# Kernel optimization log

Hardware: AMD Instinct MI355X
Metric: run time of the kernel (lower is better)

## Reference

```python
import jax, jax.numpy as jnp
import numpy as np

B, D, O = 256, 4096, 16384


def setup_inputs() -> dict:
    key = jax.random.key(0)
    k1, k2, k3, k4 = jax.random.split(key, 4)
    x1 = jax.random.normal(k1, (B, D), dtype=jnp.float32)
    x2 = jax.random.normal(k2, (B, D), dtype=jnp.float32)
    # random hash buckets in [0, O) and random +/-1 signs (homogeneous: shared by both inputs)
    h1 = jax.random.randint(k3, (D,), 0, O, dtype=jnp.int32)
    s1 = jnp.where(jax.random.uniform(k4, (D,)) < 0.5, -1.0, 1.0).astype(jnp.float32)
    return {"x1": x1, "x2": x2, "h1": h1, "s1": s1, "output_size": O}


def reference(x1, x2, h1, s1, output_size):
    # psi(): count-sketch via sign-multiply + scatter-add along feature axis
    batch = x1.shape[0]
    y1 = jnp.zeros((batch, output_size), x1.dtype).at[:, h1].add(s1 * x1)  # [B, O]
    y2 = jnp.zeros((batch, output_size), x2.dtype).at[:, h1].add(s1 * x2)  # [B, O]
    # conv(): circular convolution of the two sketches via FFT pointwise product
    out = jnp.fft.ifft(jnp.fft.fft(y1, axis=-1) * jnp.fft.fft(y2, axis=-1), axis=-1)
    return out.real.astype(x1.dtype)
```

## Files before the change

### kernel.cpp

```cpp
#include <hip/hip_runtime.h>


#define FFT_N   16384
#define LOGN    14
#define BLOCK   1024
#define DIM     4096
#define SLOT(e) ((e) ^ (((e) >> 4) & 15))
#define PI_F    3.14159265358979323846f

__device__ __forceinline__ float2 cmul(float2 a, float2 b) {
    return make_float2(a.x * b.x - a.y * b.y, a.x * b.y + a.y * b.x);
}
__device__ __forceinline__ float2 csqr(float2 a) {
    return make_float2(a.x * a.x - a.y * a.y, 2.f * a.x * a.y);
}

__device__ __forceinline__ void fft8_dif(float2* r, float phi) {
    const float CT8[4] = {1.f, 0.70710678f, 0.f, -0.70710678f};
    const float ST8[4] = {0.f, 0.70710678f, 1.f, 0.70710678f};
    float2 W[3];
    __sincosf(phi, &W[2].y, &W[2].x);
    W[1] = csqr(W[2]); W[0] = csqr(W[1]);
    #pragma unroll
    for (int p = 2; p >= 0; --p) {
        #pragma unroll
        for (int h = 0; h < 4; ++h) {
            const int jp = h & ((1 << p) - 1);
            const int j  = ((h >> p) << (p + 1)) | jp;
            const int ci = jp << (2 - p);
            const float2 T = cmul(W[p], make_float2(CT8[ci], -ST8[ci]));
            float2 a = r[j], b = r[j + (1 << p)];
            r[j] = make_float2(a.x + b.x, a.y + b.y);
            float2 d = make_float2(a.x - b.x, a.y - b.y);
            r[j + (1 << p)] = cmul(d, T);
        }
    }
}

__device__ __forceinline__ void fft8_dit(float2* r, float phi) {
    const float CT8[4] = {1.f, 0.70710678f, 0.f, -0.70710678f};
    const float ST8[4] = {0.f, 0.70710678f, 1.f, 0.70710678f};
    float2 W[3];
    __sincosf(phi, &W[2].y, &W[2].x);
    W[1] = csqr(W[2]); W[0] = csqr(W[1]);
    #pragma unroll
    for (int p = 0; p <= 2; ++p) {
        #pragma unroll
        for (int h = 0; h < 4; ++h) {
            const int jp = h & ((1 << p) - 1);
            const int j  = ((h >> p) << (p + 1)) | jp;
            const int ci = jp << (2 - p);
            const float2 T = cmul(W[p], make_float2(CT8[ci], ST8[ci]));
            float2 a = r[j];
            float2 b = cmul(r[j + (1 << p)], T);
            r[j]            = make_float2(a.x + b.x, a.y + b.y);
            r[j + (1 << p)] = make_float2(a.x - b.x, a.y - b.y);
        }
    }
}

__device__ __forceinline__ void fft4_dif(float2* r) {
    float2 a, b, d;
    a = r[0]; b = r[2]; r[0] = make_float2(a.x + b.x, a.y + b.y);
    r[2] = make_float2(a.x - b.x, a.y - b.y);
    a = r[1]; b = r[3]; r[1] = make_float2(a.x + b.x, a.y + b.y);
    d = make_float2(a.x - b.x, a.y - b.y);
    r[3] = make_float2(d.y, -d.x);
    a = r[0]; b = r[1]; r[0] = make_float2(a.x + b.x, a.y + b.y);
    r[1] = make_float2(a.x - b.x, a.y - b.y);
    a = r[2]; b = r[3]; r[2] = make_float2(a.x + b.x, a.y + b.y);
    r[3] = make_float2(a.x - b.x, a.y - b.y);
}

__device__ __forceinline__ void fft4_dit(float2* r) {
    float2 a, b;
    a = r[0]; b = r[1]; r[0] = make_float2(a.x + b.x, a.y + b.y);
    r[1] = make_float2(a.x - b.x, a.y - b.y);
    a = r[2]; b = r[3]; r[2] = make_float2(a.x + b.x, a.y + b.y);
    r[3] = make_float2(a.x - b.x, a.y - b.y);
    a = r[0]; b = r[2]; r[0] = make_float2(a.x + b.x, a.y + b.y);
    r[2] = make_float2(a.x - b.x, a.y - b.y);
    a = r[1]; b = make_float2(-r[3].y, r[3].x);
    r[1] = make_float2(a.x + b.x, a.y + b.y);
    r[3] = make_float2(a.x - b.x, a.y - b.y);
}

__device__ __forceinline__ void pass8_dif(float2* zz, int base, int slog, float phi) {
    float2 r[8];
    #pragma unroll
    for (int j = 0; j < 8; ++j) r[j] = zz[SLOT(base + (j << slog))];
    fft8_dif(r, phi);
    #pragma unroll
    for (int j = 0; j < 8; ++j) zz[SLOT(base + (j << slog))] = r[j];
}
__device__ __forceinline__ void pass8_dit(float2* zz, int base, int slog, float phi) {
    float2 r[8];
    #pragma unroll
    for (int j = 0; j < 8; ++j) r[j] = zz[SLOT(base + (j << slog))];
    fft8_dit(r, phi);
    #pragma unroll
    for (int j = 0; j < 8; ++j) zz[SLOT(base + (j << slog))] = r[j];
}

#define WAVE_FENCE() __asm__ volatile("s_waitcnt lgkmcnt(0)" ::: "memory")

__launch_bounds__(BLOCK, 4)
__global__ void cbp_fft_kernel(const float* __restrict__ x1,
                               const float* __restrict__ x2,
                               const int* __restrict__ h1,
                               const float* __restrict__ s1,
                               float* __restrict__ out) {
    __shared__ float2 zz[FFT_N];
    const int tid = threadIdx.x;
    const int b   = blockIdx.x;

    #pragma unroll
    for (int j = 0; j < 16; ++j) zz[tid + (j << 10)] = make_float2(0.f, 0.f);
    __syncthreads();

    const float* x1r = x1 + (size_t)b * DIM;
    const float* x2r = x2 + (size_t)b * DIM;
    #pragma unroll
    for (int i = 0; i < DIM / BLOCK; ++i) {
        int d = tid + i * BLOCK;
        float s = s1[d];
        int   h = h1[d];
        atomicAdd(&zz[SLOT(h)].x, s * x1r[d]);
        atomicAdd(&zz[SLOT(h)].y, s * x2r[d]);
    }
    __syncthreads();

    #pragma unroll 1
    for (int q = 0; q < 2; ++q) {
        int k = tid + (q << 10);
        pass8_dif(zz, k, 11, (float)k * (-PI_F / 8192.f));
    }
    __syncthreads();

    #pragma unroll 1
    for (int q = 0; q < 2; ++q) {
        int g = tid >> 7;
        int k = (tid & 127) + (q << 7);
        pass8_dif(zz, (g << 11) + k, 8, (float)k * (-PI_F / 1024.f));
    }
    __syncthreads();

    #pragma unroll 1
    for (int q = 0; q < 2; ++q) {
        int g = tid >> 4;
        int k = (tid & 15) + (q << 4);
        pass8_dif(zz, (g << 8) + k, 5, (float)k * (-PI_F / 128.f));
    }
    WAVE_FENCE();

    #pragma unroll 1
    for (int q = 0; q < 2; ++q) {
        int g = tid >> 1;
        int k = (tid & 1) + (q << 1);
        pass8_dif(zz, (g << 5) + k, 2, (float)k * (-PI_F / 16.f));
    }
    WAVE_FENCE();

    #pragma unroll 1
    for (int q = 0; q < 4; ++q) {
        int base = (tid << 4) + (q << 2);
        float2 r[4];
        #pragma unroll
        for (int j = 0; j < 4; ++j) r[j] = zz[SLOT(base + j)];
        fft4_dif(r);
        #pragma unroll
        for (int j = 0; j < 4; ++j) zz[SLOT(base + j)] = r[j];
    }
    __syncthreads();

    #pragma unroll
    for (int jj = 0; jj < FFT_N / BLOCK; ++jj) {
        int j  = tid + jj * BLOCK;
        int f  = (int)(__brev((unsigned)j) >> (32 - LOGN));
        int fp = (FFT_N - f) & (FFT_N - 1);
        if (f < fp) {
            int jp = (int)(__brev((unsigned)fp) >> (32 - LOGN));
            float2 a = zz[SLOT(j)];
            float2 c = zz[SLOT(jp)];
            float ar = a.x * a.x - a.y * a.y;
            float cr = c.x * c.x - c.y * c.y;
            float xr = ar - cr;
            float xi = 2.f * (a.x * a.y + c.x * c.y);
            zz[SLOT(j)]  = make_float2(0.25f * xi, -0.25f * xr);
            zz[SLOT(jp)] = make_float2(0.25f * xi,  0.25f * xr);
        } else if (f == fp) {
            float2 a = zz[SLOT(j)];
            zz[SLOT(j)] = make_float2(a.x * a.y, 0.f);
        }
    }
    __syncthreads();

    #pragma unroll 1
    for (int q = 0; q < 4; ++q) {
        int base = (tid << 4) + (q << 2);
        float2 r[4];
        #pragma unroll
        for (int j = 0; j < 4; ++j) r[j] = zz[SLOT(base + j)];
        fft4_dit(r);
        #pragma unroll
        for (int j = 0; j < 4; ++j) zz[SLOT(base + j)] = r[j];
    }
    WAVE_FENCE();

    #pragma unroll 1
    for (int q = 0; q < 2; ++q) {
        int g = tid >> 1;
        int k = (tid & 1) + (q << 1);
        pass8_dit(zz, (g << 5) + k, 2, (float)k * (PI_F / 16.f));
    }
    WAVE_FENCE();

    #pragma unroll 1
    for (int q = 0; q < 2; ++q) {
        int g = tid >> 4;
        int k = (tid & 15) + (q << 4);
        pass8_dit(zz, (g << 8) + k, 5, (float)k * (PI_F / 128.f));
    }
    __syncthreads();

    #pragma unroll 1
    for (int q = 0; q < 2; ++q) {
        int g = tid >> 7;
        int k = (tid & 127) + (q << 7);
        pass8_dit(zz, (g << 11) + k, 8, (float)k * (PI_F / 1024.f));
    }
    __syncthreads();

    float* outr = out + (size_t)b * FFT_N;
    const float inv_n = 1.0f / (float)FFT_N;
    #pragma unroll 1
    for (int q = 0; q < 2; ++q) {
        int k = tid + (q << 10);
        float2 r[8];
        #pragma unroll
        for (int j = 0; j < 8; ++j) r[j] = zz[SLOT(k + (j << 11))];
        fft8_dit(r, (float)k * (PI_F / 8192.f));
        #pragma unroll
        for (int j = 0; j < 8; ++j) outr[k + (j << 11)] = r[j].x * inv_n;
    }
}

extern "C" void kernel_launch(void* const* d_in, const int* in_sizes, int n_in,
                              void* d_out, int out_size, void* d_ws, size_t ws_size,
                              hipStream_t stream) {
    const float* x1 = (const float*)d_in[0];
    const float* x2 = (const float*)d_in[1];
    const int*   h1 = (const int*)d_in[2];
    const float* s1 = (const float*)d_in[3];
    float* out = (float*)d_out;
    const int B = in_sizes[0] / DIM;
    cbp_fft_kernel<<<B, BLOCK, 0, stream>>>(x1, x2, h1, s1, out);
}
```

Baseline: 100.1 us.

## Replace 16K complex FFT with two packed 8K real-FFT halves

Each sketch row is now packed into two 8192-point complex FFTs, with even and odd samples as real and imaginary parts, run in parallel by the two halves of the block. A post-processing step splits each transform into the real-FFT spectrum, multiplies the two spectra, and repacks the result. A single 8K inverse transform follows, and a final radix-2 twiddle stage recovers the 16K real output, written with vectorized float4 stores. This should cut butterfly work and shared-memory passes roughly in half and make the output stores coalesced. In exchange it adds extra twiddle and sincos work and the pairing logic, which is easy to get subtly wrong.

```diff
diff --git a/kernel.cpp b/kernel.cpp
--- a/kernel.cpp
+++ b/kernel.cpp
@@ -1,12 +1,13 @@
 #include <hip/hip_runtime.h>
 
 
-#define FFT_N   16384
-#define LOGN    14
+#define N1      8192
 #define BLOCK   1024
 #define DIM     4096
+#define PI_F    3.14159265358979323846f
 #define SLOT(e) ((e) ^ (((e) >> 4) & 15))
-#define PI_F    3.14159265358979323846f
+#define REV13(x) ((int)(__brev((unsigned)(x)) >> 19))
+#define WAVE_FENCE() __asm__ volatile("s_waitcnt lgkmcnt(0)" ::: "memory")
 
 __device__ __forceinline__ float2 cmul(float2 a, float2 b) {
     return make_float2(a.x * b.x - a.y * b.y, a.x * b.y + a.y * b.x);
@@ -14,6 +15,8 @@
 __device__ __forceinline__ float2 csqr(float2 a) {
     return make_float2(a.x * a.x - a.y * a.y, 2.f * a.x * a.y);
 }
+__device__ __forceinline__ float2 cadd(float2 a, float2 b) { return make_float2(a.x + b.x, a.y + b.y); }
+__device__ __forceinline__ float2 csub(float2 a, float2 b) { return make_float2(a.x - b.x, a.y - b.y); }
 
 __device__ __forceinline__ void fft8_dif(float2* r, float phi) {
     const float CT8[4] = {1.f, 0.70710678f, 0.f, -0.70710678f};
@@ -30,9 +33,8 @@
             const int ci = jp << (2 - p);
             const float2 T = cmul(W[p], make_float2(CT8[ci], -ST8[ci]));
             float2 a = r[j], b = r[j + (1 << p)];
-            r[j] = make_float2(a.x + b.x, a.y + b.y);
-            float2 d = make_float2(a.x - b.x, a.y - b.y);
-            r[j + (1 << p)] = cmul(d, T);
+            r[j] = cadd(a, b);
+            r[j + (1 << p)] = cmul(csub(a, b), T);
         }
     }
 }
@@ -53,56 +55,47 @@
             const float2 T = cmul(W[p], make_float2(CT8[ci], ST8[ci]));
             float2 a = r[j];
             float2 b = cmul(r[j + (1 << p)], T);
-            r[j]            = make_float2(a.x + b.x, a.y + b.y);
-            r[j + (1 << p)] = make_float2(a.x - b.x, a.y - b.y);
+            r[j]            = cadd(a, b);
+            r[j + (1 << p)] = csub(a, b);
         }
     }
 }
 
-__device__ __forceinline__ void fft4_dif(float2* r) {
-    float2 a, b, d;
-    a = r[0]; b = r[2]; r[0] = make_float2(a.x + b.x, a.y + b.y);
-    r[2] = make_float2(a.x - b.x, a.y - b.y);
-    a = r[1]; b = r[3]; r[1] = make_float2(a.x + b.x, a.y + b.y);
-    d = make_float2(a.x - b.x, a.y - b.y);
-    r[3] = make_float2(d.y, -d.x);
-    a = r[0]; b = r[1]; r[0] = make_float2(a.x + b.x, a.y + b.y);
-    r[1] = make_float2(a.x - b.x, a.y - b.y);
-    a = r[2]; b = r[3]; r[2] = make_float2(a.x + b.x, a.y + b.y);
-    r[3] = make_float2(a.x - b.x, a.y - b.y);
-}
-
-__device__ __forceinline__ void fft4_dit(float2* r) {
+__device__ __forceinline__ void fft4_dif_tw(float2* r, float phi) {
+    float2 W1; __sincosf(phi, &W1.y, &W1.x);
+    float2 W0 = csqr(W1);
     float2 a, b;
-    a = r[0]; b = r[1]; r[0] = make_float2(a.x + b.x, a.y + b.y);
-    r[1] = make_float2(a.x - b.x, a.y - b.y);
-    a = r[2]; b = r[3]; r[2] = make_float2(a.x + b.x, a.y + b.y);
-    r[3] = make_float2(a.x - b.x, a.y - b.y);
-    a = r[0]; b = r[2]; r[0] = make_float2(a.x + b.x, a.y + b.y);
-    r[2] = make_float2(a.x - b.x, a.y - b.y);
-    a = r[1]; b = make_float2(-r[3].y, r[3].x);
-    r[1] = make_float2(a.x + b.x, a.y + b.y);
-    r[3] = make_float2(a.x - b.x, a.y - b.y);
-}
-
-__device__ __forceinline__ void pass8_dif(float2* zz, int base, int slog, float phi) {
-    float2 r[8];
-    #pragma unroll
-    for (int j = 0; j < 8; ++j) r[j] = zz[SLOT(base + (j << slog))];
-    fft8_dif(r, phi);
-    #pragma unroll
-    for (int j = 0; j < 8; ++j) zz[SLOT(base + (j << slog))] = r[j];
-}
-__device__ __forceinline__ void pass8_dit(float2* zz, int base, int slog, float phi) {
-    float2 r[8];
-    #pragma unroll
-    for (int j = 0; j < 8; ++j) r[j] = zz[SLOT(base + (j << slog))];
-    fft8_dit(r, phi);
-    #pragma unroll
-    for (int j = 0; j < 8; ++j) zz[SLOT(base + (j << slog))] = r[j];
-}
-
-#define WAVE_FENCE() __asm__ volatile("s_waitcnt lgkmcnt(0)" ::: "memory")
+    a = r[0]; b = r[2]; r[0] = cadd(a, b); r[2] = cmul(csub(a, b), W1);
+    a = r[1]; b = r[3]; r[1] = cadd(a, b);
+    r[3] = cmul(csub(a, b), make_float2(W1.y, -W1.x));
+    a = r[0]; b = r[1]; r[0] = cadd(a, b); r[1] = cmul(csub(a, b), W0);
+    a = r[2]; b = r[3]; r[2] = cadd(a, b); r[3] = cmul(csub(a, b), W0);
+}
+
+__device__ __forceinline__ void pair_slot(float2* zz, int j) {
+    const int k  = REV13(j);
+    const int kp = (N1 - k) & (N1 - 1);
+    const int j2 = REV13(kp);
+    float2 A = zz[SLOT(j)];
+    float2 B = zz[SLOT(j2)];
+    float2 C = zz[N1 + SLOT(j)];
+    float2 D = zz[N1 + SLOT(j2)];
+    float2 E  = make_float2(0.5f * (A.x + B.x),  0.5f * (A.y - B.y));
+    float2 O  = make_float2(0.5f * (A.y + B.y), -0.5f * (A.x - B.x));
+    float2 F  = make_float2(0.5f * (C.x + D.x),  0.5f * (C.y - D.y));
+    float2 Ov = make_float2(0.5f * (C.y + D.y), -0.5f * (C.x - D.x));
+    float2 Tm; __sincosf(-PI_F * (float)k * (1.f / 8192.f), &Tm.y, &Tm.x);
+    float2 u = cmul(Tm, O);
+    float2 v = cmul(Tm, Ov);
+    float2 G = cmul(cadd(E, u), cadd(F, v));
+    float2 H = cmul(csub(E, u), csub(F, v));
+    float2 S  = make_float2(0.5f * (G.x + H.x), 0.5f * (G.y + H.y));
+    float2 gh = csub(G, H);
+    float2 t2 = cmul(make_float2(Tm.x, -Tm.y), gh);
+    float2 Dv = make_float2(-0.5f * t2.y, 0.5f * t2.x);
+    zz[SLOT(j)]  = cadd(S, Dv);
+    zz[SLOT(j2)] = make_float2(S.x - Dv.x, -(S.y - Dv.y));
+}
 
 __launch_bounds__(BLOCK, 4)
 __global__ void cbp_fft_kernel(const float* __restrict__ x1,
@@ -110,9 +103,10 @@
                                const int* __restrict__ h1,
                                const float* __restrict__ s1,
                                float* __restrict__ out) {
-    __shared__ float2 zz[FFT_N];
+    __shared__ float2 zz[2 * N1];
     const int tid = threadIdx.x;
     const int b   = blockIdx.x;
+    float* zf = (float*)zz;
 
     #pragma unroll
     for (int j = 0; j < 16; ++j) zz[tid + (j << 10)] = make_float2(0.f, 0.f);
@@ -122,126 +116,156 @@
     const float* x2r = x2 + (size_t)b * DIM;
     #pragma unroll
     for (int i = 0; i < DIM / BLOCK; ++i) {
-        int d = tid + i * BLOCK;
+        int d = tid + (i << 10);
         float s = s1[d];
         int   h = h1[d];
-        atomicAdd(&zz[SLOT(h)].x, s * x1r[d]);
-        atomicAdd(&zz[SLOT(h)].y, s * x2r[d]);
-    }
-    __syncthreads();
+        int  fi = (SLOT(h >> 1) << 1) | (h & 1);
+        atomicAdd(&zf[fi], s * x1r[d]);
+        atomicAdd(&zf[2 * N1 + fi], s * x2r[d]);
+    }
+    __syncthreads();
+
+    const int half = tid >> 9;
+    const int tt   = tid & 511;
+    float2* A = zz + half * N1;
 
     #pragma unroll 1
     for (int q = 0; q < 2; ++q) {
-        int k = tid + (q << 10);
-        pass8_dif(zz, k, 11, (float)k * (-PI_F / 8192.f));
+        int k = tt + (q << 9);
+        float2 r[8];
+        #pragma unroll
+        for (int j = 0; j < 8; ++j) r[j] = A[SLOT(k + (j << 10))];
+        fft8_dif(r, (float)k * (-PI_F / 4096.f));
+        #pragma unroll
+        for (int j = 0; j < 8; ++j) A[SLOT(k + (j << 10))] = r[j];
     }
     __syncthreads();
 
     #pragma unroll 1
     for (int q = 0; q < 2; ++q) {
-        int g = tid >> 7;
-        int k = (tid & 127) + (q << 7);
-        pass8_dif(zz, (g << 11) + k, 8, (float)k * (-PI_F / 1024.f));
-    }
-    __syncthreads();
+        int g = tt >> 6;
+        int k = (tt & 63) + (q << 6);
+        int base = (g << 10) + k;
+        float2 r[8];
+        #pragma unroll
+        for (int j = 0; j < 8; ++j) r[j] = A[SLOT(base + (j << 7))];
+        fft8_dif(r, (float)k * (-PI_F / 512.f));
+        #pragma unroll
+        for (int j = 0; j < 8; ++j) A[SLOT(base + (j << 7))] = r[j];
+    }
+    WAVE_FENCE();
 
     #pragma unroll 1
     for (int q = 0; q < 2; ++q) {
-        int g = tid >> 4;
-        int k = (tid & 15) + (q << 4);
-        pass8_dif(zz, (g << 8) + k, 5, (float)k * (-PI_F / 128.f));
-    }
-    WAVE_FENCE();
-
-    #pragma unroll 1
-    for (int q = 0; q < 2; ++q) {
-        int g = tid >> 1;
-        int k = (tid & 1) + (q << 1);
-        pass8_dif(zz, (g << 5) + k, 2, (float)k * (-PI_F / 16.f));
+        int g = tt >> 3;
+        int k = (tt & 7) + (q << 3);
+        int base = (g << 7) + k;
+        float2 r[8];
+        #pragma unroll
+        for (int j = 0; j < 8; ++j) r[j] = A[SLOT(base + (j << 4))];
+        fft8_dif(r, (float)k * (-PI_F / 64.f));
+        #pragma unroll
+        for (int j = 0; j < 8; ++j) A[SLOT(base + (j << 4))] = r[j];
+    }
+    WAVE_FENCE();
+
+    #pragma unroll 1
+    for (int k = 0; k < 4; ++k) {
+        int base = (tt << 4) + k;
+        float2 r[4];
+        #pragma unroll
+        for (int j = 0; j < 4; ++j) r[j] = A[SLOT(base + (j << 2))];
+        fft4_dif_tw(r, (float)k * (-PI_F / 8.f));
+        #pragma unroll
+        for (int j = 0; j < 4; ++j) A[SLOT(base + (j << 2))] = r[j];
     }
     WAVE_FENCE();
 
     #pragma unroll 1
     for (int q = 0; q < 4; ++q) {
-        int base = (tid << 4) + (q << 2);
+        int base = (tt << 4) + (q << 2);
         float2 r[4];
         #pragma unroll
-        for (int j = 0; j < 4; ++j) r[j] = zz[SLOT(base + j)];
-        fft4_dif(r);
-        #pragma unroll
-        for (int j = 0; j < 4; ++j) zz[SLOT(base + j)] = r[j];
-    }
-    __syncthreads();
-
-    #pragma unroll
-    for (int jj = 0; jj < FFT_N / BLOCK; ++jj) {
-        int j  = tid + jj * BLOCK;
-        int f  = (int)(__brev((unsigned)j) >> (32 - LOGN));
-        int fp = (FFT_N - f) & (FFT_N - 1);
-        if (f < fp) {
-            int jp = (int)(__brev((unsigned)fp) >> (32 - LOGN));
-            float2 a = zz[SLOT(j)];
-            float2 c = zz[SLOT(jp)];
-            float ar = a.x * a.x - a.y * a.y;
-            float cr = c.x * c.x - c.y * c.y;
-            float xr = ar - cr;
-            float xi = 2.f * (a.x * a.y + c.x * c.y);
-            zz[SLOT(j)]  = make_float2(0.25f * xi, -0.25f * xr);
-            zz[SLOT(jp)] = make_float2(0.25f * xi,  0.25f * xr);
-        } else if (f == fp) {
-            float2 a = zz[SLOT(j)];
-            zz[SLOT(j)] = make_float2(a.x * a.y, 0.f);
+        for (int j = 0; j < 4; ++j) r[j] = A[SLOT(base + j)];
+        fft4_dif_tw(r, 0.f);
+        #pragma unroll
+        for (int j = 0; j < 4; ++j) A[SLOT(base + j)] = r[j];
+    }
+    __syncthreads();
+
+    #pragma unroll 1
+    for (int i = 0; i < 4; ++i) {
+        int j = (tid + (i << 10)) << 1;
+        pair_slot(zz, j);
+    }
+    if (tid == 0) pair_slot(zz, 1);
+    __syncthreads();
+
+    {
+        int base = tid << 3;
+        float2 r[8];
+        #pragma unroll
+        for (int j = 0; j < 8; ++j) r[j] = zz[SLOT(base + j)];
+        fft8_dit(r, 0.f);
+        #pragma unroll
+        for (int j = 0; j < 8; ++j) zz[SLOT(base + j)] = r[j];
+    }
+    WAVE_FENCE();
+    {
+        int g = tid >> 3, k = tid & 7;
+        int base = (g << 6) + k;
+        float2 r[8];
+        #pragma unroll
+        for (int j = 0; j < 8; ++j) r[j] = zz[SLOT(base + (j << 3))];
+        fft8_dit(r, (float)k * (PI_F / 32.f));
+        #pragma unroll
+        for (int j = 0; j < 8; ++j) zz[SLOT(base + (j << 3))] = r[j];
+    }
+    WAVE_FENCE();
+    {
+        int g = tid >> 6, k = tid & 63;
+        int base = (g << 9) + k;
+        float2 r[8];
+        #pragma unroll
+        for (int j = 0; j < 8; ++j) r[j] = zz[SLOT(base + (j << 6))];
+        fft8_dit(r, (float)k * (PI_F / 256.f));
+        #pragma unroll
+        for (int j = 0; j < 8; ++j) zz[SLOT(base + (j << 6))] = r[j];
+    }
+    __syncthreads();
+    {
+        int g = tid >> 9, k = tid & 511;
+        int base = (g << 12) + k;
+        float2 r[8];
+        #pragma unroll
+        for (int j = 0; j < 8; ++j) r[j] = zz[SLOT(base + (j << 9))];
+        fft8_dit(r, (float)k * (PI_F / 2048.f));
+        #pragma unroll
+        for (int j = 0; j < 8; ++j) zz[SLOT(base + (j << 9))] = r[j];
+    }
+    __syncthreads();
+
+    float* outr = out + (size_t)b * (2 * N1);
+    const float inv_n1 = 1.0f / (float)N1;
+    #pragma unroll 1
+    for (int i = 0; i < 2; ++i) {
+        float2 lo[2], hi[2];
+        #pragma unroll
+        for (int s = 0; s < 2; ++s) {
+            int n = (tid << 2) + (i << 1) + s;
+            float2 a  = zz[SLOT(n)];
+            float2 bb = zz[SLOT(n + 4096)];
+            float2 T; __sincosf(PI_F * (float)n * (1.f / 4096.f), &T.y, &T.x);
+            float2 tb = cmul(T, bb);
+            lo[s] = cadd(a, tb);
+            hi[s] = csub(a, tb);
         }
-    }
-    __syncthreads();
-
-    #pragma unroll 1
-    for (int q = 0; q < 4; ++q) {
-        int base = (tid << 4) + (q << 2);
-        float2 r[4];
-        #pragma unroll
-        for (int j = 0; j < 4; ++j) r[j] = zz[SLOT(base + j)];
-        fft4_dit(r);
-        #pragma unroll
-        for (int j = 0; j < 4; ++j) zz[SLOT(base + j)] = r[j];
-    }
-    WAVE_FENCE();
-
-    #pragma unroll 1
-    for (int q = 0; q < 2; ++q) {
-        int g = tid >> 1;
-        int k = (tid & 1) + (q << 1);
-        pass8_dit(zz, (g << 5) + k, 2, (float)k * (PI_F / 16.f));
-    }
-    WAVE_FENCE();
-
-    #pragma unroll 1
-    for (int q = 0; q < 2; ++q) {
-        int g = tid >> 4;
-        int k = (tid & 15) + (q << 4);
-        pass8_dit(zz, (g << 8) + k, 5, (float)k * (PI_F / 128.f));
-    }
-    __syncthreads();
-
-    #pragma unroll 1
-    for (int q = 0; q < 2; ++q) {
-        int g = tid >> 7;
-        int k = (tid & 127) + (q << 7);
-        pass8_dit(zz, (g << 11) + k, 8, (float)k * (PI_F / 1024.f));
-    }
-    __syncthreads();
-
-    float* outr = out + (size_t)b * FFT_N;
-    const float inv_n = 1.0f / (float)FFT_N;
-    #pragma unroll 1
-    for (int q = 0; q < 2; ++q) {
-        int k = tid + (q << 10);
-        float2 r[8];
-        #pragma unroll
-        for (int j = 0; j < 8; ++j) r[j] = zz[SLOT(k + (j << 11))];
-        fft8_dit(r, (float)k * (PI_F / 8192.f));
-        #pragma unroll
-        for (int j = 0; j < 8; ++j) outr[k + (j << 11)] = r[j].x * inv_n;
+        float4 vlo = make_float4(lo[0].x * inv_n1, lo[0].y * inv_n1,
+                                 lo[1].x * inv_n1, lo[1].y * inv_n1);
+        float4 vhi = make_float4(hi[0].x * inv_n1, hi[0].y * inv_n1,
+                                 hi[1].x * inv_n1, hi[1].y * inv_n1);
+        *(float4*)(outr + (tid << 3) + (i << 2)) = vlo;
+        *(float4*)(outr + N1 + (tid << 3) + (i << 2)) = vhi;
     }
 }
 
```

Result: faster. 96.00 us (-4.1%).
